# Optimization experiments

Hardware: AMD Instinct MI355X
Metric: run time of the kernel (lower is better)

## Reference

```python
import jax, jax.numpy as jnp
import numpy as np

PAD = 4
KERNEL = 1
MAX_DISP = 4
STRIDE1 = 1
STRIDE2 = 1


def setup_inputs() -> dict:
    key = jax.random.key(0)
    k1, k2 = jax.random.split(key)
    B, C, H, W = 16, 128, 96, 160
    input1 = jax.random.normal(k1, (B, C, H, W), dtype=jnp.float32)
    input2 = jax.random.normal(k2, (B, C, H, W), dtype=jnp.float32)
    return {"input1": input1, "input2": input2}


def _correlation(input1, input2):
    # FlowNet-style patch cross-correlation (corr_multiply=1).
    # Output[b, d, y, x] = sum_{c, patch} I1[b,c,patch(y,x)] * I2[b,c,patch(y+dy,x+dx)] / (K*K*C)
    B, C, H, W = input1.shape
    kr = (KERNEL - 1) // 2  # kernel radius (0 for KERNEL=1)
    p1 = jnp.pad(input1, ((0, 0), (0, 0), (PAD, PAD), (PAD, PAD)))
    p2 = jnp.pad(input2, ((0, 0), (0, 0), (PAD, PAD), (PAD, PAD)))
    norm = jnp.float32(KERNEL * KERNEL * C)
    outs = []
    for dy in range(-MAX_DISP, MAX_DISP + 1, STRIDE2):
        for dx in range(-MAX_DISP, MAX_DISP + 1, STRIDE2):
            acc = jnp.zeros((B, H, W), dtype=input1.dtype)
            for ki in range(-kr, kr + 1):
                for kj in range(-kr, kr + 1):
                    a = p1[:, :, PAD + ki:PAD + ki + H, PAD + kj:PAD + kj + W]
                    b = p2[:, :, PAD + ki + dy:PAD + ki + dy + H,
                              PAD + kj + dx:PAD + kj + dx + W]
                    acc = acc + jnp.sum(a * b, axis=1)
            outs.append(acc / norm)
    return jnp.stack(outs, axis=1)  # [B, (2*md/s2+1)^2, H, W]


def reference(input1, input2):
    return _correlation(input1, input2)
```

## Files before the change

### kernel.cpp

```cpp
#include <hip/hip_runtime.h>
#include <stdint.h>

typedef __bf16 bf16;
typedef __attribute__((ext_vector_type(4))) __bf16 bf16x4;
typedef __attribute__((ext_vector_type(8))) __bf16 bf16x8;
typedef __attribute__((ext_vector_type(4))) float f32x4;
typedef __attribute__((ext_vector_type(4))) unsigned int u32x4;

#define W_ 160
#define H_ 96
#define C_ 128
#define B_ 16
#define HW_ (H_ * W_)
#define NXT 10
#define NYB8 12
#define NBLK (B_ * NYB8 * NXT)
#define SLICEB 10240
#define YB 40960
#define ROWSB 1536
#define CHB (16 * ROWSB)
#define LDSB (3 * CHB + 512)
#define WSSTR 1408

__device__ __forceinline__ void g2l16(const void* g, void* l) {
    __builtin_amdgcn_global_load_lds(
        (const __attribute__((address_space(1))) void*)g,
        (__attribute__((address_space(3))) void*)l, 16, 0, 0);
}

__global__ __launch_bounds__(256) void t2_kernel(const float* __restrict__ in2,
                                                 char* __restrict__ o) {
    __shared__ __align__(16) char T[40960];
    const int L   = blockIdx.x;
    const int tid = threadIdx.x;
    const float* src = in2 + (size_t)(L / H_) * C_ * HW_ + (size_t)(L % H_) * W_;
    char* dst = o + (size_t)L * YB;
    const float SC = 1.0f / 128.0f;
#pragma unroll
    for (int rd = 0; rd < 5; ++rd) {
        const int s  = rd * 256 + tid;
        const int cq = s / 40;
        const int x4 = s - cq * 40;
        const float* p = src + (size_t)(4 * cq) * HW_ + 4 * x4;
        const float4 v0 = *(const float4*)(p);
        const float4 v1 = *(const float4*)(p + HW_);
        const float4 v2 = *(const float4*)(p + 2 * HW_);
        const float4 v3 = *(const float4*)(p + 3 * HW_);
        const int oq = cq >> 1, half = cq & 1;
#pragma unroll
        for (int xj = 0; xj < 4; ++xj) {
            const int x   = 4 * x4 + xj;
            const int pos = oq ^ ((x >> 2) & 15);
            bf16x4 pk;
            pk[0] = (bf16)(((const float*)&v0)[xj] * SC);
            pk[1] = (bf16)(((const float*)&v1)[xj] * SC);
            pk[2] = (bf16)(((const float*)&v2)[xj] * SC);
            pk[3] = (bf16)(((const float*)&v3)[xj] * SC);
            *(bf16x4*)(T + x * 256 + pos * 16 + half * 8) = pk;
        }
    }
    __syncthreads();
#pragma unroll
    for (int wr = 0; wr < 10; ++wr) {
        const int s2  = wr * 256 + tid;
        const int ck  = s2 / 640;
        const int r   = s2 - ck * 640;
        const int x   = r >> 2;
        const int gsw = r & 3;
        const int gg  = gsw ^ ((x >> 1) & 3);
        const int oo  = ck * 4 + gg;
        const int pos = oo ^ ((x >> 2) & 15);
        const u32x4 v = *(const u32x4*)(T + x * 256 + pos * 16);
        *(u32x4*)(dst + (size_t)s2 * 16) = v;
    }
}

__global__ __launch_bounds__(512, 4) void corr_mfma7(const float* __restrict__ in1,
                                                     const char* __restrict__ in2t,
                                                     float* __restrict__ out) {
    __shared__ __align__(16) char Bsm[LDSB];

    const int L   = ((int)blockIdx.x & 7) * (NBLK / 8) + ((int)blockIdx.x >> 3);
    const int b   = L / (NYB8 * NXT);
    const int rem = L % (NYB8 * NXT);
    const int yb  = rem / NXT;
    const int xt  = rem % NXT;
    const int x0  = xt * 16, y0 = yb * 8;

    const int tid  = threadIdx.x;
    const int wv   = __builtin_amdgcn_readfirstlane(tid >> 6);
    const int lane = tid & 63;
    const int n    = lane & 15;
    const int g    = lane >> 4;
    const int y    = y0 + wv;

    const char* i2tb = in2t + (size_t)b * (H_ * YB);

    const float* abase = in1 + (size_t)b * C_ * HW_ + (size_t)y * W_ + (x0 + n);
    bf16x8 afrag[4];
#pragma unroll
    for (int ck = 0; ck < 4; ++ck) {
        float ar[8];
#pragma unroll
        for (int j = 0; j < 8; ++j)
            ar[j] = abase[(size_t)(ck * 32 + g * 8 + j) * HW_];
#pragma unroll
        for (int j = 0; j < 8; ++j)
            afrag[ck][j] = (bf16)ar[j];
    }
    asm volatile("s_waitcnt vmcnt(0)" ::: "memory");
    __builtin_amdgcn_sched_barrier(0);

    unsigned soff[3];
#pragma unroll
    for (int rd = 0; rd < 3; ++rd) {
        const int slot = rd * 512 + tid;
        const int row  = slot / 96;
        const int sl   = slot - row * 96;
        const int gy   = y0 - 4 + row;
        const int gy_c = min(max(gy, 0), H_ - 1);
        const int ofs  = max((x0 - 4) * 64 + sl * 16, 0);
        soff[rd] = (unsigned)(gy_c * YB + ofs);
    }

    int rboff[2];
#pragma unroll
    for (int t = 0; t < 2; ++t) {
        const int xl = n + 16 * t;
        const int sw = g ^ (((xl + 12) >> 1) & 3);
        rboff[t] = (xl * 4 + sw) * 16;
    }

    f32x4 acc[9][2];
#pragma unroll
    for (int dyi = 0; dyi < 9; ++dyi)
#pragma unroll
        for (int t = 0; t < 2; ++t)
            acc[dyi][t] = (f32x4){0.f, 0.f, 0.f, 0.f};

#define STAGE(CK, DST)                                                        \
    {                                                                         \
        const char* bck = i2tb + (CK) * SLICEB;                               \
        _Pragma("unroll")                                                     \
        for (int rd = 0; rd < 3; ++rd)                                        \
            g2l16((const void*)(bck + soff[rd]),                              \
                  (void*)((DST) + (rd * 512 + tid) * 16));                    \
    }
#define WAITB(N)                                                              \
    {                                                                         \
        asm volatile("s_waitcnt vmcnt(" #N ")" ::: "memory");                 \
        __builtin_amdgcn_s_barrier();                                         \
        __builtin_amdgcn_sched_barrier(0);                                    \
    }
#define RBAR                                                                  \
    {                                                                         \
        asm volatile("s_waitcnt lgkmcnt(0)" ::: "memory");                    \
        __builtin_amdgcn_s_barrier();                                         \
        __builtin_amdgcn_sched_barrier(0);                                    \
    }
#define COMPUTE(CK, BUF)                                                      \
    {                                                                         \
        _Pragma("unroll")                                                     \
        for (int dyi = 0; dyi < 9; ++dyi) {                                   \
            const int rowoff = (wv + dyi) * ROWSB;                            \
            _Pragma("unroll")                                                 \
            for (int t = 0; t < 2; ++t) {                                     \
                const bf16x8 bfrag =                                          \
                    *(const bf16x8*)((BUF) + rowoff + rboff[t]);              \
                acc[dyi][t] = __builtin_amdgcn_mfma_f32_16x16x32_bf16(        \
                    afrag[CK], bfrag, acc[dyi][t], 0, 0, 0);                  \
            }                                                                 \
        }                                                                     \
    }

    STAGE(0, Bsm);
    STAGE(1, Bsm + CHB);
    STAGE(2, Bsm + 2 * CHB);
    WAITB(6);
    COMPUTE(0, Bsm);
    RBAR;
    STAGE(3, Bsm);
    WAITB(6);
    COMPUTE(1, Bsm + CHB);
    WAITB(3);
    COMPUTE(2, Bsm + 2 * CHB);
    WAITB(0);
    COMPUTE(3, Bsm);
#undef STAGE
#undef WAITB
#undef RBAR
#undef COMPUTE

    __syncthreads();

    float xv[2];
#pragma unroll
    for (int t = 0; t < 2; ++t)
        xv[t] = ((unsigned)(x0 - 4 + n + 16 * t) < (unsigned)W_) ? 1.f : 0.f;
    float yv[9];
#pragma unroll
    for (int dyi = 0; dyi < 9; ++dyi)
        yv[dyi] = ((unsigned)(y - 4 + dyi) < (unsigned)H_) ? 1.f : 0.f;

    float* wsw = (float*)Bsm + wv * WSSTR;
#pragma unroll
    for (int dyi = 0; dyi < 9; ++dyi)
#pragma unroll
        for (int t = 0; t < 2; ++t)
#pragma unroll
            for (int rr = 0; rr < 4; ++rr) {
                const int m = 4 * g + rr;
                const int d = n + 16 * t - m;
                if ((unsigned)d <= 8u)
                    wsw[(dyi * 9 + d) * 17 + m] = acc[dyi][t][rr] * xv[t] * yv[dyi];
            }

    const int mm = lane & 15, rg = lane >> 4;
    const size_t ob = (size_t)(b * 81) * HW_ + (size_t)y * W_ + (x0 + mm);
#pragma unroll
    for (int q4 = 0; q4 < 20; ++q4) {
        const int rho = q4 * 4 + rg;
        out[ob + (size_t)rho * HW_] = wsw[rho * 17 + mm];
    }
    if (rg == 0)
        out[ob + (size_t)80 * HW_] = wsw[80 * 17 + mm];
}

extern "C" void kernel_launch(void* const* d_in, const int* in_sizes, int n_in,
                              void* d_out, int out_size, void* d_ws, size_t ws_size,
                              hipStream_t stream) {
    const float* in1 = (const float*)d_in[0];
    const float* in2 = (const float*)d_in[1];
    float* out = (float*)d_out;
    (void)in_sizes; (void)n_in; (void)out_size; (void)ws_size;
    char* in2t = (char*)d_ws;
    hipLaunchKernelGGL(t2_kernel, dim3(B_ * H_), dim3(256), 0, stream, in2, in2t);
    hipLaunchKernelGGL(corr_mfma7, dim3(NBLK), dim3(512), 0, stream, in1, in2t, out);
}
```

Baseline: 101.0 us.

## Split dy displacements across wave groups with 4-row tiles and double buffering

Each block now covers 4 output rows instead of 8 and uses 12 waves: each row is handled by three waves, each computing three of the nine vertical displacements. Accumulator registers per wave drop from 18 to 6 MFMA tiles, and the LDS staging changes from triple to double buffering over a 12-row window. The aim is more blocks and waves, lower register pressure and better latency hiding. The cost is more redundant loading of the A fragment and B halo rows per output row, plus extra barriers in the two-buffer schedule.

```diff
diff --git a/kernel.cpp b/kernel.cpp
--- a/kernel.cpp
+++ b/kernel.cpp
@@ -13,14 +13,14 @@
 #define B_ 16
 #define HW_ (H_ * W_)
 #define NXT 10
-#define NYB8 12
-#define NBLK (B_ * NYB8 * NXT)
+#define NYB4 24
+#define NBLK (B_ * NYB4 * NXT)
 #define SLICEB 10240
 #define YB 40960
 #define ROWSB 1536
-#define CHB (16 * ROWSB)
-#define LDSB (3 * CHB + 512)
-#define WSSTR 1408
+#define CHB (12 * ROWSB)
+#define LDSB (2 * CHB + 512)
+#define WSSTR 464
 
 __device__ __forceinline__ void g2l16(const void* g, void* l) {
     __builtin_amdgcn_global_load_lds(
@@ -75,24 +75,26 @@
     }
 }
 
-__global__ __launch_bounds__(512, 4) void corr_mfma7(const float* __restrict__ in1,
+__global__ __launch_bounds__(768, 2) void corr_mfma8(const float* __restrict__ in1,
                                                      const char* __restrict__ in2t,
                                                      float* __restrict__ out) {
     __shared__ __align__(16) char Bsm[LDSB];
 
     const int L   = ((int)blockIdx.x & 7) * (NBLK / 8) + ((int)blockIdx.x >> 3);
-    const int b   = L / (NYB8 * NXT);
-    const int rem = L % (NYB8 * NXT);
+    const int b   = L / (NYB4 * NXT);
+    const int rem = L % (NYB4 * NXT);
     const int yb  = rem / NXT;
     const int xt  = rem % NXT;
-    const int x0  = xt * 16, y0 = yb * 8;
+    const int x0  = xt * 16, y0 = yb * 4;
 
     const int tid  = threadIdx.x;
     const int wv   = __builtin_amdgcn_readfirstlane(tid >> 6);
+    const int r    = wv & 3;
+    const int G    = wv >> 2;
     const int lane = tid & 63;
     const int n    = lane & 15;
     const int g    = lane >> 4;
-    const int y    = y0 + wv;
+    const int y    = y0 + r;
 
     const char* i2tb = in2t + (size_t)b * (H_ * YB);
 
@@ -111,10 +113,10 @@
     asm volatile("s_waitcnt vmcnt(0)" ::: "memory");
     __builtin_amdgcn_sched_barrier(0);
 
-    unsigned soff[3];
-#pragma unroll
-    for (int rd = 0; rd < 3; ++rd) {
-        const int slot = rd * 512 + tid;
+    unsigned soff[2];
+#pragma unroll
+    for (int rd = 0; rd < 2; ++rd) {
+        const int slot = rd * 768 + tid;
         const int row  = slot / 96;
         const int sl   = slot - row * 96;
         const int gy   = y0 - 4 + row;
@@ -131,24 +133,31 @@
         rboff[t] = (xl * 4 + sw) * 16;
     }
 
-    f32x4 acc[9][2];
-#pragma unroll
-    for (int dyi = 0; dyi < 9; ++dyi)
+    f32x4 acc[3][2];
+#pragma unroll
+    for (int j = 0; j < 3; ++j)
 #pragma unroll
         for (int t = 0; t < 2; ++t)
-            acc[dyi][t] = (f32x4){0.f, 0.f, 0.f, 0.f};
+            acc[j][t] = (f32x4){0.f, 0.f, 0.f, 0.f};
 
 #define STAGE(CK, DST)                                                        \
     {                                                                         \
         const char* bck = i2tb + (CK) * SLICEB;                               \
-        _Pragma("unroll")                                                     \
-        for (int rd = 0; rd < 3; ++rd)                                        \
-            g2l16((const void*)(bck + soff[rd]),                              \
-                  (void*)((DST) + (rd * 512 + tid) * 16));                    \
-    }
-#define WAITB(N)                                                              \
-    {                                                                         \
-        asm volatile("s_waitcnt vmcnt(" #N ")" ::: "memory");                 \
+        g2l16((const void*)(bck + soff[0]), (void*)((DST) + tid * 16));       \
+        if (wv < 6)                                                           \
+            g2l16((const void*)(bck + soff[1]),                               \
+                  (void*)((DST) + (768 + tid) * 16));                         \
+    }
+#define WAITC1                                                                \
+    {                                                                         \
+        if (wv < 6) { asm volatile("s_waitcnt vmcnt(2)" ::: "memory"); }      \
+        else        { asm volatile("s_waitcnt vmcnt(1)" ::: "memory"); }      \
+        __builtin_amdgcn_s_barrier();                                         \
+        __builtin_amdgcn_sched_barrier(0);                                    \
+    }
+#define WAITC0                                                                \
+    {                                                                         \
+        asm volatile("s_waitcnt vmcnt(0)" ::: "memory");                      \
         __builtin_amdgcn_s_barrier();                                         \
         __builtin_amdgcn_sched_barrier(0);                                    \
     }
@@ -161,33 +170,35 @@
 #define COMPUTE(CK, BUF)                                                      \
     {                                                                         \
         _Pragma("unroll")                                                     \
-        for (int dyi = 0; dyi < 9; ++dyi) {                                   \
-            const int rowoff = (wv + dyi) * ROWSB;                            \
+        for (int j = 0; j < 3; ++j) {                                         \
+            const int rowoff = (r + 3 * G + j) * ROWSB;                       \
             _Pragma("unroll")                                                 \
             for (int t = 0; t < 2; ++t) {                                     \
                 const bf16x8 bfrag =                                          \
                     *(const bf16x8*)((BUF) + rowoff + rboff[t]);              \
-                acc[dyi][t] = __builtin_amdgcn_mfma_f32_16x16x32_bf16(        \
-                    afrag[CK], bfrag, acc[dyi][t], 0, 0, 0);                  \
+                acc[j][t] = __builtin_amdgcn_mfma_f32_16x16x32_bf16(          \
+                    afrag[CK], bfrag, acc[j][t], 0, 0, 0);                    \
             }                                                                 \
         }                                                                     \
     }
 
     STAGE(0, Bsm);
     STAGE(1, Bsm + CHB);
-    STAGE(2, Bsm + 2 * CHB);
-    WAITB(6);
+    WAITC1;
     COMPUTE(0, Bsm);
     RBAR;
-    STAGE(3, Bsm);
-    WAITB(6);
+    STAGE(2, Bsm);
+    WAITC1;
     COMPUTE(1, Bsm + CHB);
-    WAITB(3);
-    COMPUTE(2, Bsm + 2 * CHB);
-    WAITB(0);
-    COMPUTE(3, Bsm);
+    RBAR;
+    STAGE(3, Bsm + CHB);
+    WAITC1;
+    COMPUTE(2, Bsm);
+    WAITC0;
+    COMPUTE(3, Bsm + CHB);
 #undef STAGE
-#undef WAITB
+#undef WAITC1
+#undef WAITC0
 #undef RBAR
 #undef COMPUTE
 
@@ -197,14 +208,14 @@
 #pragma unroll
     for (int t = 0; t < 2; ++t)
         xv[t] = ((unsigned)(x0 - 4 + n + 16 * t) < (unsigned)W_) ? 1.f : 0.f;
-    float yv[9];
-#pragma unroll
-    for (int dyi = 0; dyi < 9; ++dyi)
-        yv[dyi] = ((unsigned)(y - 4 + dyi) < (unsigned)H_) ? 1.f : 0.f;
+    float yv[3];
+#pragma unroll
+    for (int j = 0; j < 3; ++j)
+        yv[j] = ((unsigned)(y - 4 + 3 * G + j) < (unsigned)H_) ? 1.f : 0.f;
 
     float* wsw = (float*)Bsm + wv * WSSTR;
 #pragma unroll
-    for (int dyi = 0; dyi < 9; ++dyi)
+    for (int j = 0; j < 3; ++j)
 #pragma unroll
         for (int t = 0; t < 2; ++t)
 #pragma unroll
@@ -212,18 +223,20 @@
                 const int m = 4 * g + rr;
                 const int d = n + 16 * t - m;
                 if ((unsigned)d <= 8u)
-                    wsw[(dyi * 9 + d) * 17 + m] = acc[dyi][t][rr] * xv[t] * yv[dyi];
+                    wsw[(j * 9 + d) * 17 + m] = acc[j][t][rr] * xv[t] * yv[j];
             }
 
     const int mm = lane & 15, rg = lane >> 4;
-    const size_t ob = (size_t)(b * 81) * HW_ + (size_t)y * W_ + (x0 + mm);
-#pragma unroll
-    for (int q4 = 0; q4 < 20; ++q4) {
-        const int rho = q4 * 4 + rg;
-        out[ob + (size_t)rho * HW_] = wsw[rho * 17 + mm];
-    }
-    if (rg == 0)
-        out[ob + (size_t)80 * HW_] = wsw[80 * 17 + mm];
+    const size_t ob = (size_t)(b * 81 + 27 * G) * HW_ + (size_t)y * W_ + (x0 + mm);
+#pragma unroll
+    for (int q4 = 0; q4 < 6; ++q4) {
+        const int l = q4 * 4 + rg;
+        out[ob + (size_t)l * HW_] = wsw[l * 17 + mm];
+    }
+    if (rg < 3) {
+        const int l = 24 + rg;
+        out[ob + (size_t)l * HW_] = wsw[l * 17 + mm];
+    }
 }
 
 extern "C" void kernel_launch(void* const* d_in, const int* in_sizes, int n_in,
@@ -235,5 +248,5 @@
     (void)in_sizes; (void)n_in; (void)out_size; (void)ws_size;
     char* in2t = (char*)d_ws;
     hipLaunchKernelGGL(t2_kernel, dim3(B_ * H_), dim3(256), 0, stream, in2, in2t);
-    hipLaunchKernelGGL(corr_mfma7, dim3(NBLK), dim3(512), 0, stream, in1, in2t, out);
-}
+    hipLaunchKernelGGL(corr_mfma8, dim3(NBLK), dim3(768), 0, stream, in1, in2t, out);
+}
```

Result: slower. 122.4 us (+21.2%).

## Shrink correlation tile to 4 rows per block with double-buffered staging

Applied to the files above, without the earlier changes.

Each block of the correlation kernel now covers 4 output rows instead of 8, using 256 threads, so twice as many blocks are launched. The shared-memory staging goes from three buffers to two, each sized for a 12-row window. The channel-chunk pipeline is rebuilt as alternating double buffers, with per-wave wait counts because the fifth load is issued by only two waves. The smaller shared-memory and thread footprint is meant to allow more resident blocks and better load balance, at the cost of more redundant halo-row loads per output row (12 rows staged for 4 outputs instead of 16 for 8).

```diff
diff --git a/kernel.cpp b/kernel.cpp
--- a/kernel.cpp
+++ b/kernel.cpp
@@ -13,13 +13,13 @@
 #define B_ 16
 #define HW_ (H_ * W_)
 #define NXT 10
-#define NYB8 12
-#define NBLK (B_ * NYB8 * NXT)
+#define NYB4 24
+#define NBLK (B_ * NYB4 * NXT)
 #define SLICEB 10240
 #define YB 40960
 #define ROWSB 1536
-#define CHB (16 * ROWSB)
-#define LDSB (3 * CHB + 512)
+#define CHB (12 * ROWSB)
+#define LDSB (2 * CHB + 512)
 #define WSSTR 1408
 
 __device__ __forceinline__ void g2l16(const void* g, void* l) {
@@ -75,17 +75,17 @@
     }
 }
 
-__global__ __launch_bounds__(512, 4) void corr_mfma7(const float* __restrict__ in1,
+__global__ __launch_bounds__(256, 4) void corr_mfma9(const float* __restrict__ in1,
                                                      const char* __restrict__ in2t,
                                                      float* __restrict__ out) {
     __shared__ __align__(16) char Bsm[LDSB];
 
     const int L   = ((int)blockIdx.x & 7) * (NBLK / 8) + ((int)blockIdx.x >> 3);
-    const int b   = L / (NYB8 * NXT);
-    const int rem = L % (NYB8 * NXT);
+    const int b   = L / (NYB4 * NXT);
+    const int rem = L % (NYB4 * NXT);
     const int yb  = rem / NXT;
     const int xt  = rem % NXT;
-    const int x0  = xt * 16, y0 = yb * 8;
+    const int x0  = xt * 16, y0 = yb * 4;
 
     const int tid  = threadIdx.x;
     const int wv   = __builtin_amdgcn_readfirstlane(tid >> 6);
@@ -111,10 +111,10 @@
     asm volatile("s_waitcnt vmcnt(0)" ::: "memory");
     __builtin_amdgcn_sched_barrier(0);
 
-    unsigned soff[3];
-#pragma unroll
-    for (int rd = 0; rd < 3; ++rd) {
-        const int slot = rd * 512 + tid;
+    unsigned soff[5];
+#pragma unroll
+    for (int rd = 0; rd < 5; ++rd) {
+        const int slot = rd * 256 + tid;
         const int row  = slot / 96;
         const int sl   = slot - row * 96;
         const int gy   = y0 - 4 + row;
@@ -141,14 +141,24 @@
 #define STAGE(CK, DST)                                                        \
     {                                                                         \
         const char* bck = i2tb + (CK) * SLICEB;                               \
-        _Pragma("unroll")                                                     \
-        for (int rd = 0; rd < 3; ++rd)                                        \
-            g2l16((const void*)(bck + soff[rd]),                              \
-                  (void*)((DST) + (rd * 512 + tid) * 16));                    \
-    }
-#define WAITB(N)                                                              \
-    {                                                                         \
-        asm volatile("s_waitcnt vmcnt(" #N ")" ::: "memory");                 \
+        g2l16((const void*)(bck + soff[0]), (void*)((DST) + tid * 16));       \
+        g2l16((const void*)(bck + soff[1]), (void*)((DST) + (256 + tid) * 16)); \
+        g2l16((const void*)(bck + soff[2]), (void*)((DST) + (512 + tid) * 16)); \
+        g2l16((const void*)(bck + soff[3]), (void*)((DST) + (768 + tid) * 16)); \
+        if (wv < 2)                                                           \
+            g2l16((const void*)(bck + soff[4]),                               \
+                  (void*)((DST) + (1024 + tid) * 16));                        \
+    }
+#define WAITC                                                                 \
+    {                                                                         \
+        if (wv < 2) { asm volatile("s_waitcnt vmcnt(5)" ::: "memory"); }      \
+        else        { asm volatile("s_waitcnt vmcnt(4)" ::: "memory"); }      \
+        __builtin_amdgcn_s_barrier();                                         \
+        __builtin_amdgcn_sched_barrier(0);                                    \
+    }
+#define WAIT0                                                                 \
+    {                                                                         \
+        asm volatile("s_waitcnt vmcnt(0)" ::: "memory");                      \
         __builtin_amdgcn_s_barrier();                                         \
         __builtin_amdgcn_sched_barrier(0);                                    \
     }
@@ -175,19 +185,21 @@
 
     STAGE(0, Bsm);
     STAGE(1, Bsm + CHB);
-    STAGE(2, Bsm + 2 * CHB);
-    WAITB(6);
+    WAITC;
     COMPUTE(0, Bsm);
     RBAR;
-    STAGE(3, Bsm);
-    WAITB(6);
+    STAGE(2, Bsm);
+    WAITC;
     COMPUTE(1, Bsm + CHB);
-    WAITB(3);
-    COMPUTE(2, Bsm + 2 * CHB);
-    WAITB(0);
-    COMPUTE(3, Bsm);
+    RBAR;
+    STAGE(3, Bsm + CHB);
+    WAITC;
+    COMPUTE(2, Bsm);
+    WAIT0;
+    COMPUTE(3, Bsm + CHB);
 #undef STAGE
-#undef WAITB
+#undef WAITC
+#undef WAIT0
 #undef RBAR
 #undef COMPUTE
 
@@ -235,5 +247,5 @@
     (void)in_sizes; (void)n_in; (void)out_size; (void)ws_size;
     char* in2t = (char*)d_ws;
     hipLaunchKernelGGL(t2_kernel, dim3(B_ * H_), dim3(256), 0, stream, in2, in2t);
-    hipLaunchKernelGGL(corr_mfma7, dim3(NBLK), dim3(512), 0, stream, in1, in2t, out);
-}
+    hipLaunchKernelGGL(corr_mfma9, dim3(NBLK), dim3(256), 0, stream, in1, in2t, out);
+}
```

After: 103.8 us. +2.7%, slower.
